# Performance work log

Measured on AMD Instinct MI355X. Metric: run time of the kernel, lower is better.

The kernel has to match this reference:

```python
import jax, jax.numpy as jnp
import numpy as np

N = 20000          # total atoms
NPG = 40           # atoms per molecule
G = N // NPG       # 500 graphs
DEG = 16           # neighbors per atom
E = N * DEG        # 320000 edges
HID = 128
NF = 128           # num_filters == num Gaussians
CUTOFF = 10.0
L = 3
IN_DIM = 100
LOG2 = 0.6931471805599453


def ssp(x):
    # ShiftedSoftplus: softplus(x) - log(2)
    return jax.nn.softplus(x) - LOG2


def setup_inputs() -> dict:
    key = jax.random.key(0)
    ks = jax.random.split(key, 16)
    rng = np.random.default_rng(0)

    # within-graph random edges, no self loops (mimics radius_graph structure)
    src = np.repeat(np.arange(N), DEG)
    base = (src // NPG) * NPG
    dst = base + (src - base + 1 + rng.integers(0, NPG - 1, size=E)) % NPG
    edge_index = jnp.asarray(np.stack([src, dst]).astype(np.int32))

    box = CUTOFF / np.sqrt(3.0)  # all pairwise distances < cutoff
    pos = jax.random.uniform(ks[0], (N, 3), dtype=jnp.float32) * box
    z = jax.random.randint(ks[1], (N,), 0, IN_DIM, dtype=jnp.int32)
    batch = jnp.asarray((np.arange(N) // NPG).astype(np.int32))

    s = 0.05
    emb = jax.random.normal(ks[2], (IN_DIM, HID), dtype=jnp.float32) * s
    mlp_w1 = jax.random.normal(ks[3], (L, NF, NF), dtype=jnp.float32) * s
    mlp_b1 = jnp.zeros((L, NF), jnp.float32)
    mlp_w2 = jax.random.normal(ks[4], (L, NF, NF), dtype=jnp.float32) * s
    mlp_b2 = jnp.zeros((L, NF), jnp.float32)
    cf_w1 = jax.random.normal(ks[5], (L, HID, NF), dtype=jnp.float32) * s   # no bias
    cf_w2 = jax.random.normal(ks[6], (L, NF, HID), dtype=jnp.float32) * s
    cf_b2 = jnp.zeros((L, HID), jnp.float32)
    lin_w = jax.random.normal(ks[7], (L, HID, HID), dtype=jnp.float32) * s
    lin_b = jnp.zeros((L, HID), jnp.float32)
    head_w1 = jax.random.normal(ks[8], (HID, HID // 2), dtype=jnp.float32) * s
    head_b1 = jnp.zeros((HID // 2,), jnp.float32)
    head_w2 = jax.random.normal(ks[9], (HID // 2, 1), dtype=jnp.float32) * s
    head_b2 = jnp.zeros((1,), jnp.float32)

    return dict(pos=pos, emb=emb, mlp_w1=mlp_w1, mlp_b1=mlp_b1, mlp_w2=mlp_w2,
                mlp_b2=mlp_b2, cf_w1=cf_w1, cf_w2=cf_w2, cf_b2=cf_b2,
                lin_w=lin_w, lin_b=lin_b, head_w1=head_w1, head_b1=head_b1,
                head_w2=head_w2, head_b2=head_b2, z=z, batch=batch,
                edge_index=edge_index)


def reference(pos, emb, mlp_w1, mlp_b1, mlp_w2, mlp_b2, cf_w1, cf_w2, cf_b2,
              lin_w, lin_b, head_w1, head_b1, head_w2, head_b2,
              z, batch, edge_index):
    row, col = edge_index[0], edge_index[1]  # source j, target i (PyG flow)
    d = jnp.linalg.norm(pos[row] - pos[col], axis=-1)  # [E]

    # Gaussian smearing
    offset = jnp.linspace(0.0, CUTOFF, NF)
    coeff = -0.5 / (offset[1] - offset[0]) ** 2
    edge_attr = jnp.exp(coeff * (d[:, None] - offset) ** 2)  # [E, NF]

    # cosine cutoff
    C = 0.5 * (jnp.cos(d * jnp.pi / CUTOFF) + 1.0)  # [E]

    h = emb[z]  # [N, HID]
    for l in range(L):
        # edge filter MLP
        Wf = ssp(edge_attr @ mlp_w1[l] + mlp_b1[l]) @ mlp_w2[l] + mlp_b2[l]
        Wf = Wf * C[:, None]                       # [E, NF]
        x1 = h @ cf_w1[l]                          # [N, NF]
        msg = x1[row] * Wf                         # gather + per-edge filter
        agg = jax.ops.segment_sum(msg, col, num_segments=N)  # scatter-add
        x = ssp(agg @ cf_w2[l] + cf_b2[l])
        x = x @ lin_w[l] + lin_b[l]
        h = h + x

    y = ssp(h @ head_w1 + head_b1) @ head_w2 + head_b2   # [N, 1]
    out = jax.ops.segment_sum(y, batch, num_segments=G).squeeze(-1)  # [G]
    return out
```

## Files before the change

kernel.cpp:

```cpp
#include <hip/hip_runtime.h>
#include <math.h>

#define N_ATOMS 20000
#define G_GRAPHS 500
#define NPG 40
#define DEG 16
#define E_EDGES (N_ATOMS * DEG)
#define EPM (NPG * DEG)
#define EPAD 680
#define HID 128
#define NF 128
#define TBL2 80
#define TROWS (TBL2 + 2)
#define PROWS 81
#define CUTOFF 10.0f
#define LOG2F_ 0.6931471805599453f

typedef __attribute__((ext_vector_type(8))) short short8v;
typedef __attribute__((ext_vector_type(4))) float f32x4;
typedef __attribute__((ext_vector_type(2))) __bf16 bf16x2;
typedef unsigned short ushort_t;

__device__ __forceinline__ float ssp_f(float x) {
  float ax = fabsf(x);
  return fmaxf(x, 0.0f) + log1pf(expf(-ax)) - LOG2F_;
}
__device__ __forceinline__ ushort_t bf16rne(float x) {
  __bf16 b = (__bf16)x;
  return __builtin_bit_cast(ushort_t, b);
}
__device__ __forceinline__ unsigned pk2(float a, float b) {
  return (unsigned)bf16rne(a) | ((unsigned)bf16rne(b) << 16);
}
__device__ __forceinline__ float bflo(unsigned u) { return __uint_as_float(u << 16); }
__device__ __forceinline__ float bfhi(unsigned u) { return __uint_as_float(u & 0xFFFF0000u); }
__device__ __forceinline__ int bidx(int row, int col) {
  return row * 128 + (col ^ ((row & 7) << 3));
}
__device__ __forceinline__ float fdot2b(unsigned a, unsigned b, float c) {
#if defined(__has_builtin) && __has_builtin(__builtin_amdgcn_fdot2_f32_bf16)
  return __builtin_amdgcn_fdot2_f32_bf16(__builtin_bit_cast(bf16x2, a),
                                         __builtin_bit_cast(bf16x2, b), c, false);
#else
  return fmaf(bflo(a), bflo(b), fmaf(bfhi(a), bfhi(b), c));
#endif
}

__global__ void __launch_bounds__(512) k_pre(
    const float* __restrict__ mlp_w1, const float* __restrict__ mlp_b1,
    const float* __restrict__ mlp_w2, const float* __restrict__ mlp_b2,
    const float* __restrict__ cf_w1, const float* __restrict__ cf_w2,
    const float* __restrict__ lin_w, const float* __restrict__ hw1,
    const float* __restrict__ pos, const int* __restrict__ ei,
    unsigned* __restrict__ ptabg, ushort_t* __restrict__ wtb,
    uint4* __restrict__ ge, int* __restrict__ gstart) {
  int b = blockIdx.x;
  int t = threadIdx.x;

  if (b < 33) {
    __shared__ float eaT[NF][8];
    __shared__ float hvT[NF][8];
    int l = b / 11;
    int rbase = (b % 11) * 8;
    const float* w1 = mlp_w1 + (size_t)l * NF * NF;
    const float* b1 = mlp_b1 + (size_t)l * NF;
    const float* w2 = mlp_w2 + (size_t)l * NF * NF;
    const float* b2 = mlp_b2 + (size_t)l * NF;
    ushort_t* pp = (ushort_t*)(ptabg + (size_t)l * PROWS * 128);
    const float hh = CUTOFF / (float)(TBL2 - 1);
    const float delta = CUTOFF / (float)(NF - 1);
    const float coeff = -0.5f / (delta * delta);
    int j = t & 127;
    bool act = t < 128;
    if (act) {
#pragma unroll
      for (int rr = 0; rr < 8; ++rr) {
        float d = ((float)(rbase + rr) - 1.0f) * hh;
        float tt = d - delta * (float)j;
        eaT[j][rr] = expf(coeff * tt * tt);
      }
    }
    __syncthreads();
    float acc[8], wreg[16];
    if (act) {
      float b1j = b1[j];
#pragma unroll
      for (int rr = 0; rr < 8; ++rr) acc[rr] = b1j;
      for (int kb = 0; kb < NF; kb += 16) {
#pragma unroll
        for (int i = 0; i < 16; ++i) wreg[i] = w1[(kb + i) * NF + j];
#pragma unroll
        for (int i = 0; i < 16; ++i) {
          float4 e0 = *(const float4*)&eaT[kb + i][0];
          float4 e1 = *(const float4*)&eaT[kb + i][4];
          float wv = wreg[i];
          acc[0] = fmaf(e0.x, wv, acc[0]); acc[1] = fmaf(e0.y, wv, acc[1]);
          acc[2] = fmaf(e0.z, wv, acc[2]); acc[3] = fmaf(e0.w, wv, acc[3]);
          acc[4] = fmaf(e1.x, wv, acc[4]); acc[5] = fmaf(e1.y, wv, acc[5]);
          acc[6] = fmaf(e1.z, wv, acc[6]); acc[7] = fmaf(e1.w, wv, acc[7]);
        }
      }
#pragma unroll
      for (int rr = 0; rr < 8; ++rr) hvT[j][rr] = ssp_f(acc[rr]);
    }
    __syncthreads();
    if (act) {
      float b2j = b2[j];
#pragma unroll
      for (int rr = 0; rr < 8; ++rr) acc[rr] = b2j;
      for (int kb = 0; kb < NF; kb += 16) {
#pragma unroll
        for (int i = 0; i < 16; ++i) wreg[i] = w2[(kb + i) * NF + j];
#pragma unroll
        for (int i = 0; i < 16; ++i) {
          float4 e0 = *(const float4*)&hvT[kb + i][0];
          float4 e1 = *(const float4*)&hvT[kb + i][4];
          float wv = wreg[i];
          acc[0] = fmaf(e0.x, wv, acc[0]); acc[1] = fmaf(e0.y, wv, acc[1]);
          acc[2] = fmaf(e0.z, wv, acc[2]); acc[3] = fmaf(e0.w, wv, acc[3]);
          acc[4] = fmaf(e1.x, wv, acc[4]); acc[5] = fmaf(e1.y, wv, acc[5]);
          acc[6] = fmaf(e1.z, wv, acc[6]); acc[7] = fmaf(e1.w, wv, acc[7]);
        }
      }
#pragma unroll
      for (int rr = 0; rr < 8; ++rr) {
        int s = rbase + rr;
        if (s < TROWS) {
          float d = ((float)s - 1.0f) * hh;
          float C = 0.5f * (cosf(d * (float)M_PI / CUTOFF) + 1.0f);
          ushort_t v = bf16rne(acc[rr] * C);
          if (s < PROWS) pp[(s * 128 + j) * 2] = v;
          if (s >= 1) pp[((s - 1) * 128 + j) * 2 + 1] = v;
        }
      }
    }
  } else if (b < 71) {
    __shared__ float tile[32][33];
    int pb = b - 33;
    int tr = (t & 255) >> 5, tc = t & 31;
    bool act = t < 256;
    if (pb < 36) {
      int m = pb >> 2, tj = pb & 3;
      int l = m / 3, ty = m % 3;
      const float* src = (ty == 0 ? cf_w1 : ty == 1 ? cf_w2 : lin_w) + (size_t)l * 128 * 128;
      ushort_t* dst = wtb + (size_t)m * 128 * 128;
      for (int ti = 0; ti < 4; ++ti) {
        __syncthreads();
        if (act) {
#pragma unroll
          for (int i = 0; i < 4; ++i) {
            int r = tr + i * 8;
            tile[r][tc] = src[(ti * 32 + r) * 128 + tj * 32 + tc];
          }
        }
        __syncthreads();
        if (act) {
#pragma unroll
          for (int i = 0; i < 4; ++i) {
            int r = tr + i * 8;
            dst[(tj * 32 + r) * 128 + ti * 32 + tc] = bf16rne(tile[tc][r]);
          }
        }
      }
    } else {
      int tj = pb - 36;
      ushort_t* dst = wtb + (size_t)9 * 128 * 128;
      for (int ti = 0; ti < 4; ++ti) {
        __syncthreads();
        if (act) {
#pragma unroll
          for (int i = 0; i < 4; ++i) {
            int r = tr + i * 8;
            tile[r][tc] = hw1[(ti * 32 + r) * 64 + tj * 32 + tc];
          }
        }
        __syncthreads();
        if (act) {
#pragma unroll
          for (int i = 0; i < 4; ++i) {
            int r = tr + i * 8;
            dst[(tj * 32 + r) * 128 + ti * 32 + tc] = bf16rne(tile[tc][r]);
          }
        }
      }
    }
  } else {
    __shared__ float spos[NPG * 3];
    __shared__ int cnt[NPG];
    __shared__ int pfx[NPG + 1];
    __shared__ uint4 epk[EPM];
    __shared__ unsigned char ecol[EPM];
    __shared__ short ssidx[EPAD];
    int g = b - 71, a0 = g * NPG;
    if (t < NPG * 3) spos[t] = pos[a0 * 3 + t];
    if (t < NPG) cnt[t] = 0;
    for (int i = t; i < EPAD; i += 512) ssidx[i] = -1;
    __syncthreads();
    int ebase = a0 * DEG;
    const float tscale = (float)(TBL2 - 1) / CUTOFF;
    for (int i = t; i < EPM; i += 512) {
      int r = ei[ebase + i] - a0;
      int c = ei[E_EDGES + ebase + i] - a0;
      float dx = spos[3 * r + 0] - spos[3 * c + 0];
      float dy = spos[3 * r + 1] - spos[3 * c + 1];
      float dz = spos[3 * r + 2] - spos[3 * c + 2];
      float ft = sqrtf(dx * dx + dy * dy + dz * dz) * tscale;
      int i0 = min((int)ft, TBL2 - 2);
      float tt = ft - (float)i0;
      float t2 = tt * tt, t3 = t2 * tt;
      float w0 = 0.5f * (-t3 + 2.f * t2 - tt);
      float w1 = 0.5f * (3.f * t3 - 5.f * t2 + 2.f);
      float w2 = 0.5f * (-3.f * t3 + 4.f * t2 + tt);
      float w3 = 0.5f * (t3 - t2);
      epk[i] = make_uint4(pk2(w0, w1), pk2(w2, w3), (unsigned)(i0 << 7),
                          (unsigned)((r << 6) | (((r & 7) << 2) << 16)));
      ecol[i] = (unsigned char)c;
      atomicAdd(&cnt[c], 1);
    }
    __syncthreads();
    if (t == 0) {
      int s = 0;
      for (int a = 0; a < NPG; ++a) { pfx[a] = s; s += (cnt[a] + 1) & ~1; }
      pfx[NPG] = s;
    }
    __syncthreads();
    int w = t >> 6, lane = t & 63;
    for (int a = w * 5; a < w * 5 + 5; ++a) {
      int p = pfx[a];
#pragma unroll
      for (int ch = 0; ch < EPM / 64; ++ch) {
        int e = ch * 64 + lane;
        bool match = ((int)ecol[e] == a);
        unsigned long long bal = __ballot(match);
        if (match) ssidx[p + __popcll(bal & ((1ull << lane) - 1ull))] = (short)e;
        p += __popcll(bal);
      }
    }
    __syncthreads();
    int ptot = pfx[NPG];
    const uint4 z4 = make_uint4(0u, 0u, 0u, 0u);
    for (int i = t; i < ptot; i += 512) {
      int e = ssidx[i];
      ge[(size_t)g * EPAD + i] = (e >= 0) ? epk[e] : z4;
    }
    if (t <= NPG) gstart[g * (NPG + 1) + t] = pfx[t];
  }
}

__global__ void __launch_bounds__(512) k_mol(
    const float* __restrict__ emb, const int* __restrict__ z,
    const uint4* __restrict__ ge, const int* __restrict__ gstart,
    const unsigned* __restrict__ ptabg, const ushort_t* __restrict__ wtb,
    const float* __restrict__ cf_b2, const float* __restrict__ lin_b,
    const float* __restrict__ hb1, const float* __restrict__ hw2,
    const float* __restrict__ hb2, float* __restrict__ out) {
  __shared__ unsigned ptab[PROWS * 128];
  __shared__ ushort_t sb0[48 * 128];
  __shared__ ushort_t sb1[48 * 128];
  __shared__ uint4 sedge[EPAD];
  __shared__ int sstart[NPG + 1];
  __shared__ float shead[48];
  int g = blockIdx.x, a0 = g * NPG, t = threadIdx.x;
  int w = t >> 6, l6 = t & 63, r15 = l6 & 15, q = l6 >> 4;
  int colo = w * 16 + r15;
  int half = l6 >> 5, li = l6 & 31, ch0 = li * 4;

  int ptot = gstart[g * (NPG + 1) + NPG];
  {
    if (t <= NPG) sstart[t] = gstart[g * (NPG + 1) + t];
    const uint4* gsrc = ge + (size_t)g * EPAD;
    for (int i = t; i < ptot; i += 512) sedge[i] = gsrc[i];
    if (t < 48) shead[t] = 0.f;
    ((unsigned*)sb0)[40 * 64 + t] = 0u;
    ((unsigned*)sb1)[40 * 64 + t] = 0u;
    const uint4* tg4 = (const uint4*)ptabg;
    uint4* st4 = (uint4*)ptab;
    for (int i = t; i < PROWS * 32; i += 512) st4[i] = tg4[i];
  }
  float hreg[12];
#pragma unroll
  for (int mt = 0; mt < 3; ++mt) {
#pragma unroll
    for (int r = 0; r < 4; ++r) {
      int row = mt * 16 + q * 4 + r;
      float v = 0.f;
      if (row < NPG) {
        v = emb[(size_t)z[a0 + row] * HID + colo];
        sb0[bidx(row, colo)] = bf16rne(v);
      }
      hreg[mt * 4 + r] = v;
    }
  }
  __syncthreads();

  for (int l = 0; l < 3; ++l) {
    const ushort_t* w1t = wtb + (size_t)(l * 3 + 0) * 128 * 128;
    const ushort_t* w2t = wtb + (size_t)(l * 3 + 1) * 128 * 128;
    const ushort_t* lwt = wtb + (size_t)(l * 3 + 2) * 128 * 128;
    if (l > 0) {
      const uint4* tg4 = (const uint4*)(ptabg + (size_t)l * PROWS * 128);
      uint4* st4 = (uint4*)ptab;
      for (int i = t; i < PROWS * 32; i += 512) st4[i] = tg4[i];
    }
    {
      short8v bfr[4];
      const ushort_t* wp = w1t + (size_t)colo * 128 + q * 8;
#pragma unroll
      for (int ks = 0; ks < 4; ++ks) bfr[ks] = *(const short8v*)(wp + ks * 32);
#pragma unroll
      for (int mt = 0; mt < 3; ++mt) {
        f32x4 acc = (f32x4){0.f, 0.f, 0.f, 0.f};
#pragma unroll
        for (int ks = 0; ks < 4; ++ks) {
          short8v af = *(const short8v*)&sb0[bidx(mt * 16 + r15, ks * 32 + q * 8)];
          acc = __builtin_amdgcn_mfma_f32_16x16x32_bf16(af, bfr[ks], acc, 0, 0, 0);
        }
#pragma unroll
        for (int r = 0; r < 4; ++r) sb1[bidx(mt * 16 + q * 4 + r, colo)] = bf16rne(acc[r]);
      }
    }
    __syncthreads();
    {
      const unsigned* b1u = (const unsigned*)sb1;
      unsigned* b0u = (unsigned*)sb0;
      for (int a = w; a < NPG; a += 8) {
        int kb = sstart[a], ke = sstart[a + 1];
        float a0c = 0.f, a1c = 0.f, a2c = 0.f, a3c = 0.f;
        for (int k = kb + half; k < ke; k += 2) {
          uint4 ev = sedge[k];
          const unsigned* tb = ptab + ev.z + ch0;
          uint4 pa = *(const uint4*)tb;
          uint4 pb = *(const uint4*)(tb + 256);
          uint2 xv = *(const uint2*)&b1u[(ev.w & 0xffffu) + ((li * 2) ^ (ev.w >> 16))];
          float f0 = fdot2b(ev.x, pa.x, 0.f); f0 = fdot2b(ev.y, pb.x, f0);
          float f1 = fdot2b(ev.x, pa.y, 0.f); f1 = fdot2b(ev.y, pb.y, f1);
          float f2 = fdot2b(ev.x, pa.z, 0.f); f2 = fdot2b(ev.y, pb.z, f2);
          float f3 = fdot2b(ev.x, pa.w, 0.f); f3 = fdot2b(ev.y, pb.w, f3);
          a0c = fmaf(bflo(xv.x), f0, a0c);
          a1c = fmaf(bfhi(xv.x), f1, a1c);
          a2c = fmaf(bflo(xv.y), f2, a2c);
          a3c = fmaf(bfhi(xv.y), f3, a3c);
        }
        a0c += __shfl_xor(a0c, 32);
        a1c += __shfl_xor(a1c, 32);
        a2c += __shfl_xor(a2c, 32);
        a3c += __shfl_xor(a3c, 32);
        if (half == 0) {
          uint2 o;
          o.x = pk2(a0c, a1c);
          o.y = pk2(a2c, a3c);
          *(uint2*)&b0u[(a << 6) + ((li * 2) ^ ((a & 7) << 2))] = o;
        }
      }
    }
    __syncthreads();
    {
      float bc = cf_b2[(size_t)l * HID + colo];
      short8v bfr[4];
      const ushort_t* wp = w2t + (size_t)colo * 128 + q * 8;
#pragma unroll
      for (int ks = 0; ks < 4; ++ks) bfr[ks] = *(const short8v*)(wp + ks * 32);
#pragma unroll
      for (int mt = 0; mt < 3; ++mt) {
        f32x4 acc = (f32x4){0.f, 0.f, 0.f, 0.f};
#pragma unroll
        for (int ks = 0; ks < 4; ++ks) {
          short8v af = *(const short8v*)&sb0[bidx(mt * 16 + r15, ks * 32 + q * 8)];
          acc = __builtin_amdgcn_mfma_f32_16x16x32_bf16(af, bfr[ks], acc, 0, 0, 0);
        }
#pragma unroll
        for (int r = 0; r < 4; ++r) {
          int row = mt * 16 + q * 4 + r;
          float v = (row < NPG) ? ssp_f(acc[r] + bc) : 0.f;
          sb1[bidx(row, colo)] = bf16rne(v);
        }
      }
    }
    __syncthreads();
    {
      float bc = lin_b[(size_t)l * HID + colo];
      short8v bfr[4];
      const ushort_t* wp = lwt + (size_t)colo * 128 + q * 8;
#pragma unroll
      for (int ks = 0; ks < 4; ++ks) bfr[ks] = *(const short8v*)(wp + ks * 32);
#pragma unroll
      for (int mt = 0; mt < 3; ++mt) {
        f32x4 acc = (f32x4){0.f, 0.f, 0.f, 0.f};
#pragma unroll
        for (int ks = 0; ks < 4; ++ks) {
          short8v af = *(const short8v*)&sb1[bidx(mt * 16 + r15, ks * 32 + q * 8)];
          acc = __builtin_amdgcn_mfma_f32_16x16x32_bf16(af, bfr[ks], acc, 0, 0, 0);
        }
#pragma unroll
        for (int r = 0; r < 4; ++r) {
          int row = mt * 16 + q * 4 + r;
          if (row < NPG) {
            float nh = hreg[mt * 4 + r] + acc[r] + bc;
            hreg[mt * 4 + r] = nh;
            sb0[bidx(row, colo)] = bf16rne(nh);
          }
        }
      }
    }
    __syncthreads();
  }

  {
    const ushort_t* h1t = wtb + (size_t)9 * 128 * 128;
    for (int tile = w; tile < 12; tile += 8) {
      int mt = tile >> 2, nt = tile & 3;
      int col = nt * 16 + r15;
      short8v bfr[4];
      const ushort_t* wp = h1t + (size_t)col * 128 + q * 8;
#pragma unroll
      for (int ks = 0; ks < 4; ++ks) bfr[ks] = *(const short8v*)(wp + ks * 32);
      f32x4 acc = (f32x4){0.f, 0.f, 0.f, 0.f};
#pragma unroll
      for (int ks = 0; ks < 4; ++ks) {
        short8v af = *(const short8v*)&sb0[bidx(mt * 16 + r15, ks * 32 + q * 8)];
        acc = __builtin_amdgcn_mfma_f32_16x16x32_bf16(af, bfr[ks], acc, 0, 0, 0);
      }
      float hb = hb1[col];
      float w2v = hw2[col];
#pragma unroll
      for (int r = 0; r < 4; ++r) {
        int row = mt * 16 + q * 4 + r;
        float y = ssp_f(acc[r] + hb) * w2v;
        y += __shfl_xor(y, 1);
        y += __shfl_xor(y, 2);
        y += __shfl_xor(y, 4);
        y += __shfl_xor(y, 8);
        if (r15 == 0 && row < NPG) atomicAdd(&shead[row], y);
      }
    }
  }
  __syncthreads();
  if (w == 0) {
    float v = (l6 < NPG) ? shead[l6] : 0.f;
#pragma unroll
    for (int off = 32; off; off >>= 1) v += __shfl_xor(v, off);
    if (l6 == 0) out[g] = v + (float)NPG * hb2[0];
  }
}

extern "C" void kernel_launch(void* const* d_in, const int* in_sizes, int n_in,
                              void* d_out, int out_size, void* d_ws, size_t ws_size,
                              hipStream_t stream) {
  const float* pos    = (const float*)d_in[0];
  const float* emb    = (const float*)d_in[1];
  const float* mlp_w1 = (const float*)d_in[2];
  const float* mlp_b1 = (const float*)d_in[3];
  const float* mlp_w2 = (const float*)d_in[4];
  const float* mlp_b2 = (const float*)d_in[5];
  const float* cf_w1  = (const float*)d_in[6];
  const float* cf_w2  = (const float*)d_in[7];
  const float* cf_b2  = (const float*)d_in[8];
  const float* lin_w  = (const float*)d_in[9];
  const float* lin_b  = (const float*)d_in[10];
  const float* hw1    = (const float*)d_in[11];
  const float* hb1    = (const float*)d_in[12];
  const float* hw2    = (const float*)d_in[13];
  const float* hb2    = (const float*)d_in[14];
  const int*   z      = (const int*)d_in[15];
  const int*   ei     = (const int*)d_in[17];

  char* wsb = (char*)d_ws;
  uint4*    ge     = (uint4*)wsb;
  int*      gstart = (int*)(wsb + 5440000);
  unsigned* ptabg  = (unsigned*)(wsb + 5522000);
  ushort_t* wtb    = (ushort_t*)(wsb + 5646416);
  size_t need = 5646416 + 327680;
  if (ws_size < need) return;

  k_pre<<<571, 512, 0, stream>>>(mlp_w1, mlp_b1, mlp_w2, mlp_b2, cf_w1, cf_w2, lin_w,
                                 hw1, pos, ei, ptabg, wtb, ge, gstart);
  k_mol<<<G_GRAPHS, 512, 0, stream>>>(emb, z, ge, gstart, ptabg, wtb,
                                      cf_b2, lin_b, hb1, hw2, hb2, (float*)d_out);
}
```

Measured before the change: 102.9 us.

## Fuse per-molecule edge preprocessing into the main molecule kernel

Moves the per-graph edge distance, spline-weight packing and destination-sorting work from the precompute kernel into k_mol. Each molecule block now builds its sorted edge list directly in shared memory, reusing the sb0/sb1 buffers as scratch. This removes the global round trip through the ge/gstart workspace and shrinks k_pre to 71 blocks. The trade-off is extra serial work and more barriers at the start of each k_mol block, which k_pre previously ran in parallel across 500 separate blocks.

```diff
diff --git a/kernel.cpp b/kernel.cpp
--- a/kernel.cpp
+++ b/kernel.cpp
@@ -51,9 +51,7 @@
     const float* __restrict__ mlp_w2, const float* __restrict__ mlp_b2,
     const float* __restrict__ cf_w1, const float* __restrict__ cf_w2,
     const float* __restrict__ lin_w, const float* __restrict__ hw1,
-    const float* __restrict__ pos, const int* __restrict__ ei,
-    unsigned* __restrict__ ptabg, ushort_t* __restrict__ wtb,
-    uint4* __restrict__ ge, int* __restrict__ gstart) {
+    unsigned* __restrict__ ptabg, ushort_t* __restrict__ wtb) {
   int b = blockIdx.x;
   int t = threadIdx.x;
 
@@ -134,7 +132,7 @@
         }
       }
     }
-  } else if (b < 71) {
+  } else {
     __shared__ float tile[32][33];
     int pb = b - 33;
     int tr = (t & 255) >> 5, tc = t & 31;
@@ -184,18 +182,44 @@
         }
       }
     }
-  } else {
-    __shared__ float spos[NPG * 3];
-    __shared__ int cnt[NPG];
-    __shared__ int pfx[NPG + 1];
-    __shared__ uint4 epk[EPM];
-    __shared__ unsigned char ecol[EPM];
-    __shared__ short ssidx[EPAD];
-    int g = b - 71, a0 = g * NPG;
+  }
+}
+
+__global__ void __launch_bounds__(512) k_mol(
+    const float* __restrict__ emb, const int* __restrict__ z,
+    const float* __restrict__ pos, const int* __restrict__ ei,
+    const unsigned* __restrict__ ptabg, const ushort_t* __restrict__ wtb,
+    const float* __restrict__ cf_b2, const float* __restrict__ lin_b,
+    const float* __restrict__ hb1, const float* __restrict__ hw2,
+    const float* __restrict__ hb2, float* __restrict__ out) {
+  __shared__ unsigned ptab[PROWS * 128];
+  __shared__ __align__(16) ushort_t sb0[48 * 128];
+  __shared__ __align__(16) ushort_t sb1[48 * 128];
+  __shared__ uint4 sedge[EPAD];
+  __shared__ int sstart[NPG + 1];
+  __shared__ float shead[48];
+  __shared__ float spos[NPG * 3];
+  __shared__ int scnt[NPG];
+  __shared__ unsigned char secol[EPM];
+  int g = blockIdx.x, a0 = g * NPG, t = threadIdx.x;
+  int w = t >> 6, l6 = t & 63, r15 = l6 & 15, q = l6 >> 4;
+  int colo = w * 16 + r15;
+  int half = l6 >> 5, li = l6 & 31, ch0 = li * 4;
+
+  uint4* epk = (uint4*)sb0;
+  short* ssidx = (short*)sb1;
+
+  {
+    const uint4* tg4 = (const uint4*)ptabg;
+    uint4* st4 = (uint4*)ptab;
+    for (int i = t; i < PROWS * 32; i += 512) st4[i] = tg4[i];
     if (t < NPG * 3) spos[t] = pos[a0 * 3 + t];
-    if (t < NPG) cnt[t] = 0;
+    if (t < NPG) scnt[t] = 0;
+    if (t < 48) shead[t] = 0.f;
     for (int i = t; i < EPAD; i += 512) ssidx[i] = -1;
-    __syncthreads();
+  }
+  __syncthreads();
+  {
     int ebase = a0 * DEG;
     const float tscale = (float)(TBL2 - 1) / CUTOFF;
     for (int i = t; i < EPM; i += 512) {
@@ -214,69 +238,40 @@
       float w3 = 0.5f * (t3 - t2);
       epk[i] = make_uint4(pk2(w0, w1), pk2(w2, w3), (unsigned)(i0 << 7),
                           (unsigned)((r << 6) | (((r & 7) << 2) << 16)));
-      ecol[i] = (unsigned char)c;
-      atomicAdd(&cnt[c], 1);
-    }
-    __syncthreads();
-    if (t == 0) {
-      int s = 0;
-      for (int a = 0; a < NPG; ++a) { pfx[a] = s; s += (cnt[a] + 1) & ~1; }
-      pfx[NPG] = s;
-    }
-    __syncthreads();
-    int w = t >> 6, lane = t & 63;
+      secol[i] = (unsigned char)c;
+      atomicAdd(&scnt[c], 1);
+    }
+  }
+  __syncthreads();
+  if (t == 0) {
+    int s = 0;
+    for (int a = 0; a < NPG; ++a) { sstart[a] = s; s += (scnt[a] + 1) & ~1; }
+    sstart[NPG] = s;
+  }
+  __syncthreads();
+  {
     for (int a = w * 5; a < w * 5 + 5; ++a) {
-      int p = pfx[a];
+      int p = sstart[a];
 #pragma unroll
       for (int ch = 0; ch < EPM / 64; ++ch) {
-        int e = ch * 64 + lane;
-        bool match = ((int)ecol[e] == a);
+        int e = ch * 64 + l6;
+        bool match = ((int)secol[e] == a);
         unsigned long long bal = __ballot(match);
-        if (match) ssidx[p + __popcll(bal & ((1ull << lane) - 1ull))] = (short)e;
+        if (match) ssidx[p + __popcll(bal & ((1ull << l6) - 1ull))] = (short)e;
         p += __popcll(bal);
       }
     }
-    __syncthreads();
-    int ptot = pfx[NPG];
-    const uint4 z4 = make_uint4(0u, 0u, 0u, 0u);
+  }
+  __syncthreads();
+  {
+    int ptot = sstart[NPG];
+    const uint4 zz = make_uint4(0u, 0u, 0u, 0u);
     for (int i = t; i < ptot; i += 512) {
       int e = ssidx[i];
-      ge[(size_t)g * EPAD + i] = (e >= 0) ? epk[e] : z4;
-    }
-    if (t <= NPG) gstart[g * (NPG + 1) + t] = pfx[t];
-  }
-}
-
-__global__ void __launch_bounds__(512) k_mol(
-    const float* __restrict__ emb, const int* __restrict__ z,
-    const uint4* __restrict__ ge, const int* __restrict__ gstart,
-    const unsigned* __restrict__ ptabg, const ushort_t* __restrict__ wtb,
-    const float* __restrict__ cf_b2, const float* __restrict__ lin_b,
-    const float* __restrict__ hb1, const float* __restrict__ hw2,
-    const float* __restrict__ hb2, float* __restrict__ out) {
-  __shared__ unsigned ptab[PROWS * 128];
-  __shared__ ushort_t sb0[48 * 128];
-  __shared__ ushort_t sb1[48 * 128];
-  __shared__ uint4 sedge[EPAD];
-  __shared__ int sstart[NPG + 1];
-  __shared__ float shead[48];
-  int g = blockIdx.x, a0 = g * NPG, t = threadIdx.x;
-  int w = t >> 6, l6 = t & 63, r15 = l6 & 15, q = l6 >> 4;
-  int colo = w * 16 + r15;
-  int half = l6 >> 5, li = l6 & 31, ch0 = li * 4;
-
-  int ptot = gstart[g * (NPG + 1) + NPG];
-  {
-    if (t <= NPG) sstart[t] = gstart[g * (NPG + 1) + t];
-    const uint4* gsrc = ge + (size_t)g * EPAD;
-    for (int i = t; i < ptot; i += 512) sedge[i] = gsrc[i];
-    if (t < 48) shead[t] = 0.f;
-    ((unsigned*)sb0)[40 * 64 + t] = 0u;
-    ((unsigned*)sb1)[40 * 64 + t] = 0u;
-    const uint4* tg4 = (const uint4*)ptabg;
-    uint4* st4 = (uint4*)ptab;
-    for (int i = t; i < PROWS * 32; i += 512) st4[i] = tg4[i];
-  }
+      sedge[i] = (e >= 0) ? epk[e] : zz;
+    }
+  }
+  __syncthreads();
   float hreg[12];
 #pragma unroll
   for (int mt = 0; mt < 3; ++mt) {
@@ -291,6 +286,7 @@
       hreg[mt * 4 + r] = v;
     }
   }
+  ((unsigned*)sb0)[40 * 64 + t] = 0u;
   __syncthreads();
 
   for (int l = 0; l < 3; ++l) {
@@ -465,15 +461,13 @@
   const int*   ei     = (const int*)d_in[17];
 
   char* wsb = (char*)d_ws;
-  uint4*    ge     = (uint4*)wsb;
-  int*      gstart = (int*)(wsb + 5440000);
-  unsigned* ptabg  = (unsigned*)(wsb + 5522000);
-  ushort_t* wtb    = (ushort_t*)(wsb + 5646416);
-  size_t need = 5646416 + 327680;
+  unsigned* ptabg = (unsigned*)wsb;
+  ushort_t* wtb   = (ushort_t*)(wsb + 124416);
+  size_t need = 124416 + 327680;
   if (ws_size < need) return;
 
-  k_pre<<<571, 512, 0, stream>>>(mlp_w1, mlp_b1, mlp_w2, mlp_b2, cf_w1, cf_w2, lin_w,
-                                 hw1, pos, ei, ptabg, wtb, ge, gstart);
-  k_mol<<<G_GRAPHS, 512, 0, stream>>>(emb, z, ge, gstart, ptabg, wtb,
+  k_pre<<<71, 512, 0, stream>>>(mlp_w1, mlp_b1, mlp_w2, mlp_b2, cf_w1, cf_w2, lin_w,
+                                hw1, ptabg, wtb);
+  k_mol<<<G_GRAPHS, 512, 0, stream>>>(emb, z, pos, ei, ptabg, wtb,
                                       cf_b2, lin_b, hb1, hw2, hb2, (float*)d_out);
 }
```

Result: no change. 104.2 us (+1.3%).
